# Kernel optimization log

Hardware: AMD Instinct MI355X
Metric: run time of the kernel (lower is better)

## Reference

```python
import jax, jax.numpy as jnp
import numpy as np

N_NODES = 50000
N_EDGES = 800000
FEAT_IN = 128
POS_IN = 16
EDGE_FEAT_IN = 16
H = 64
L = 4


def _lin(k, fan_in, fan_out):
    kw, kb = jax.random.split(k)
    s = 1.0 / np.sqrt(fan_in)
    W = jax.random.uniform(kw, (fan_in, fan_out), minval=-s, maxval=s, dtype=jnp.float32)
    b = jax.random.uniform(kb, (fan_out,), minval=-s, maxval=s, dtype=jnp.float32)
    return W, b


def setup_inputs() -> dict:
    key = jax.random.key(0)
    ks = jax.random.split(key, 32)
    h = jax.random.normal(ks[0], (N_NODES, FEAT_IN), dtype=jnp.float32)
    e = jax.random.normal(ks[1], (N_EDGES, EDGE_FEAT_IN), dtype=jnp.float32)
    p = jax.random.normal(ks[2], (N_NODES, POS_IN), dtype=jnp.float32)
    edge_index = jax.random.randint(ks[3], (2, N_EDGES), 0, N_NODES, dtype=jnp.int64 if jax.config.x64_enabled else jnp.int32)
    he_W, he_b = _lin(ks[4], FEAT_IN, H)
    ee_W, ee_b = _lin(ks[5], EDGE_FEAT_IN, H)
    pe_W, pe_b = _lin(ks[6], POS_IN, H)

    def stack(fan_in, base):
        Ws, bs = [], []
        for i in range(L):
            W, b = _lin(jax.random.fold_in(ks[7], base * 100 + i), fan_in, H)
            Ws.append(W); bs.append(b)
        return jnp.stack(Ws), jnp.stack(bs)

    hm_W, hm_b = stack(5 * H, 0)  # h_message_mlp
    hu_W, hu_b = stack(2 * H, 1)  # h_update
    eu_W, eu_b = stack(3 * H, 2)  # e_update
    pm_W, pm_b = stack(3 * H, 3)  # p_message_mlp
    pu_W, pu_b = stack(2 * H, 4)  # p_update
    return dict(h=h, e=e, p=p, edge_index=edge_index,
                he_W=he_W, he_b=he_b, ee_W=ee_W, ee_b=ee_b, pe_W=pe_W, pe_b=pe_b,
                hm_W=hm_W, hm_b=hm_b, hu_W=hu_W, hu_b=hu_b,
                eu_W=eu_W, eu_b=eu_b, pm_W=pm_W, pm_b=pm_b, pu_W=pu_W, pu_b=pu_b)


def reference(h, e, p, edge_index, he_W, he_b, ee_W, ee_b, pe_W, pe_b,
              hm_W, hm_b, hu_W, hu_b, eu_W, eu_b, pm_W, pm_b, pu_W, pu_b):
    send, rec = edge_index[0], edge_index[1]
    n = h.shape[0]
    h = h @ he_W + he_b  # [N,H]
    e = e @ ee_W + ee_b  # [E,H]
    p = p @ pe_W + pe_b  # [N,H]
    for i in range(L):
        hp_send = jnp.concatenate((h[send], p[send]), axis=1)  # [E,2H]
        hp_rec = jnp.concatenate((h[rec], p[rec]), axis=1)     # [E,2H]
        h_msg = jnp.concatenate((hp_send, hp_rec, e), axis=1) @ hm_W[i] + hm_b[i]  # [E,H]
        h_agg = jax.ops.segment_sum(h_msg, rec, num_segments=n)  # [N,H]
        h = jnp.concatenate((h, h_agg), axis=1) @ hu_W[i] + hu_b[i]
        e = jnp.concatenate((h[send], h[rec], e), axis=1) @ eu_W[i] + eu_b[i]
        p_msg = jnp.concatenate((p[send], p[rec], e), axis=1) @ pm_W[i] + pm_b[i]
        p_agg = jax.ops.segment_sum(p_msg, rec, num_segments=n)
        p = jnp.concatenate((p, p_agg), axis=1) @ pu_W[i] + pu_b[i]
    return (h, p)
```

## Files before the change

kernel.cpp:

```cpp
#include <hip/hip_runtime.h>
#include <hip/hip_bf16.h>

#define NN 50000
#define NE 800000

typedef __hip_bfloat16 bf16;
typedef __attribute__((ext_vector_type(8))) short bf16x8s;
typedef __attribute__((ext_vector_type(4))) float f32x4;

#define OFF_HP     0L
#define OFF_HSUM   12800000L
#define OFF_PSUM   25600000L
#define OFF_ESUM   38400000L
#define OFF_EAGGA  41600000L
#define OFF_EAGGB  54400000L
#define OFF_WFMT   67200000L
#define OFF_ROWPTR 67716096L
#define OFF_COLIDX 67916100L
#define OFF_SSEND  71116100L
#define OFF_SEG    74316100L
#define OFF_CNT    77516100L
#define OFF_BSUM   77716100L

#define SCAN_B 196

#define FW_HE 0
#define FW_EE 8192
#define FW_PE 10240
#define FW_L0 12288
#define LSTR  61440
#define R_HAGG 0
#define R_HMR  12288
#define R_HU   20480
#define R_EUS  28672
#define R_EUR  32768
#define R_EUE  36864
#define R_PAGG 40960
#define R_PMR  49152
#define R_PU   53248

#define AGG_STRIDE 72

__device__ __forceinline__ bf16x8s bfrag(const bf16* w, int c, int t, int lane) {
    return *(const bf16x8s*)(w + ((long)(c*4 + t)*64 + lane)*8);
}
__device__ __forceinline__ bf16x8s cvt8(const float* fp) {
    float4 f0 = ((const float4*)fp)[0];
    float4 f1 = ((const float4*)fp)[1];
    bf16 tmp[8];
    tmp[0]=__float2bfloat16(f0.x); tmp[1]=__float2bfloat16(f0.y);
    tmp[2]=__float2bfloat16(f0.z); tmp[3]=__float2bfloat16(f0.w);
    tmp[4]=__float2bfloat16(f1.x); tmp[5]=__float2bfloat16(f1.y);
    tmp[6]=__float2bfloat16(f1.z); tmp[7]=__float2bfloat16(f1.w);
    return *(const bf16x8s*)tmp;
}

__global__ __launch_bounds__(256) void wfmt_k(
    const float* __restrict__ he, const float* __restrict__ ee, const float* __restrict__ pe,
    const float* __restrict__ hm, const float* __restrict__ hu, const float* __restrict__ eu,
    const float* __restrict__ pm, const float* __restrict__ pu, bf16* __restrict__ wf)
{
    int s = blockIdx.x;
    const float* src = nullptr; int rowoff = 0, Ksrc = 0, Kpad = 0, mode = 0, split = 0, gap = 0; long doff = 0;
    if      (s == 0) { src = he; Ksrc = 128; Kpad = 128; doff = FW_HE; }
    else if (s == 1) { src = ee; Ksrc = 16;  Kpad = 32;  doff = FW_EE; }
    else if (s == 2) { src = pe; Ksrc = 16;  Kpad = 32;  doff = FW_PE; }
    else {
        int i = (s - 3) / 9, g = (s - 3) % 9;
        long base = FW_L0 + (long)i*LSTR;
        const float* HM = hm + (long)i*320*64;
        const float* HU = hu + (long)i*128*64;
        const float* EU = eu + (long)i*192*64;
        const float* PM = pm + (long)i*192*64;
        const float* PU = pu + (long)i*128*64;
        switch (g) {
          case 0:  src=HM; mode=4; split=128; gap=128; Kpad=192; doff=base+R_HAGG; break;
          case 1:  src=HM; rowoff=128; Ksrc=128; Kpad=128; doff=base+R_HMR;  break;
          case 2:  src=HU; rowoff=0;   Ksrc=128; Kpad=128; doff=base+R_HU;   break;
          case 3:  src=EU; rowoff=0;   Ksrc=64;  Kpad=64;  doff=base+R_EUS;  break;
          case 4:  src=EU; rowoff=64;  Ksrc=64;  Kpad=64;  doff=base+R_EUR;  break;
          case 5:  src=EU; rowoff=128; Ksrc=64;  Kpad=64;  doff=base+R_EUE;  break;
          case 6:  src=PM; mode=4; split=64; gap=64; Kpad=128; doff=base+R_PAGG; break;
          case 7:  src=PM; rowoff=64;  Ksrc=64;  Kpad=64;  doff=base+R_PMR;  break;
          default: src=PU; rowoff=0;   Ksrc=128; Kpad=128; doff=base+R_PU;   break;
        }
    }
    int total = Kpad * 64;
    for (int idx = threadIdx.x; idx < total; idx += 256) {
        int j = idx & 7, l = (idx >> 3) & 63, ct = idx >> 9;
        int c = ct >> 2, t = ct & 3;
        int k = c*32 + (l >> 4)*8 + j;
        int n = t*16 + (l & 15);
        float v;
        if (mode == 4) v = src[(long)(k + (k >= split ? gap : 0))*64 + n];
        else           v = (k < Ksrc) ? src[(long)(rowoff + k)*64 + n] : 0.f;
        wf[doff + idx] = __float2bfloat16(v);
    }
}

__global__ __launch_bounds__(256) void hist_k(const int* __restrict__ rec, int* __restrict__ cnt)
{
    int e = blockIdx.x*256 + threadIdx.x;
    if (e < NE) atomicAdd(&cnt[rec[e]], 1);
}

__global__ __launch_bounds__(256) void scan1_k(const int* __restrict__ cnt, int* __restrict__ bsum)
{
    __shared__ int sdata[256];
    int tid = threadIdx.x;
    int i = blockIdx.x*256 + tid;
    sdata[tid] = (i < NN) ? cnt[i] : 0;
    __syncthreads();
    #pragma unroll
    for (int off = 128; off > 0; off >>= 1) {
        if (tid < off) sdata[tid] += sdata[tid + off];
        __syncthreads();
    }
    if (tid == 0) bsum[blockIdx.x] = sdata[0];
}

__global__ __launch_bounds__(256) void scan2_k(int* __restrict__ bsum)
{
    __shared__ int sdata[256];
    int tid = threadIdx.x;
    int v = (tid < SCAN_B) ? bsum[tid] : 0;
    sdata[tid] = v;
    __syncthreads();
    #pragma unroll
    for (int off = 1; off < 256; off <<= 1) {
        int t = (tid >= off) ? sdata[tid - off] : 0;
        __syncthreads();
        sdata[tid] += t;
        __syncthreads();
    }
    if (tid < SCAN_B) bsum[tid] = sdata[tid] - v;
}

__global__ __launch_bounds__(256) void scan3_k(const int* __restrict__ cnt,
    const int* __restrict__ bsum, int* __restrict__ rowptr)
{
    __shared__ int sdata[256];
    int tid = threadIdx.x;
    int i = blockIdx.x*256 + tid;
    sdata[tid] = (i < NN) ? cnt[i] : 0;
    __syncthreads();
    #pragma unroll
    for (int off = 1; off < 256; off <<= 1) {
        int t = (tid >= off) ? sdata[tid - off] : 0;
        __syncthreads();
        sdata[tid] += t;
        __syncthreads();
    }
    if (i < NN) rowptr[i + 1] = sdata[tid] + bsum[blockIdx.x];
    if (i == 0) rowptr[0] = 0;
}

__global__ __launch_bounds__(256) void scatter_k(const int* __restrict__ rec,
    const int* __restrict__ rowptr, int* __restrict__ cursor, int* __restrict__ colidx)
{
    int e = blockIdx.x*256 + threadIdx.x;
    if (e < NE) {
        int r = rec[e];
        int pos = atomicAdd(&cursor[r], 1);
        colidx[rowptr[r] + pos] = e;
    }
}

__global__ __launch_bounds__(256) void segfill_k(const int* __restrict__ rowptr, int* __restrict__ seg)
{
    int n = blockIdx.x*256 + threadIdx.x;
    if (n < NN) {
        int b = rowptr[n], e = rowptr[n + 1];
        for (int j = b; j < e; ++j) seg[j] = n;
    }
}

template <int DEPTH, bool BOTH>
__global__ __launch_bounds__(256) void gsum64_k(const bf16* __restrict__ hp, int coff,
    const int* __restrict__ ssend, const int* __restrict__ seg,
    float* __restrict__ out1, float* __restrict__ out2)
{
    __shared__ int s_ids[256];
    __shared__ int s_seg[256];
    int tid = threadIdx.x, lane = tid & 63, wv = tid >> 6;
    int gbase = blockIdx.x*256;
    s_ids[tid] = ssend[gbase + tid];
    s_seg[tid] = seg[gbase + tid];
    __syncthreads();
    int j0 = wv*64;
    const bf16* base = hp + coff + lane;
    constexpr int NB = 64 / DEPTH;

    unsigned short va[DEPTH], vb[DEPTH];
    unsigned short wa[BOTH ? DEPTH : 1], wb[BOTH ? DEPTH : 1];
    #pragma unroll
    for (int k = 0; k < DEPTH; ++k) {
        long o = (long)s_ids[j0 + k]*128;
        va[k] = *(const unsigned short*)(base + o);
        if (BOTH) wa[k] = *(const unsigned short*)(base + o + 64);
    }

    float a = 0.f, b2 = 0.f;
    int cur = s_seg[j0];
    #pragma unroll
    for (int b = 0; b < NB; ++b) {
        if (b < NB - 1) {
            #pragma unroll
            for (int k = 0; k < DEPTH; ++k) {
                long o = (long)s_ids[j0 + (b+1)*DEPTH + k]*128;
                vb[k] = *(const unsigned short*)(base + o);
                if (BOTH) wb[k] = *(const unsigned short*)(base + o + 64);
            }
        }
        #pragma unroll
        for (int k = 0; k < DEPTH; ++k) {
            int n = s_seg[j0 + b*DEPTH + k];
            if (n != cur) {
                atomicAdd(&out1[(long)cur*64 + lane], a);
                if (BOTH) atomicAdd(&out2[(long)cur*64 + lane], b2);
                a = 0.f; b2 = 0.f; cur = n;
            }
            a += __uint_as_float(((unsigned)va[k]) << 16);
            if (BOTH) b2 += __uint_as_float(((unsigned)wa[k]) << 16);
        }
        if (b < NB - 1) {
            #pragma unroll
            for (int k = 0; k < DEPTH; ++k) { va[k] = vb[k]; if (BOTH) wa[k] = wb[k]; }
        }
    }
    atomicAdd(&out1[(long)cur*64 + lane], a);
    if (BOTH) atomicAdd(&out2[(long)cur*64 + lane], b2);
}

__global__ __launch_bounds__(256) void esum_k(const float* __restrict__ e_in,
    const int* __restrict__ colidx, const int* __restrict__ seg, const int* __restrict__ send,
    int* __restrict__ ssend, float* __restrict__ esum)
{
    __shared__ int s_ids[256];
    __shared__ int s_seg[256];
    int tid = threadIdx.x;
    int gbase = blockIdx.x*256;
    int id = colidx[gbase + tid];
    s_ids[tid] = id;
    s_seg[tid] = seg[gbase + tid];
    ssend[gbase + tid] = send[id];
    __syncthreads();
    int grp = tid >> 4, c = tid & 15;
    int j0 = grp*16;
    float vv[16];
    #pragma unroll
    for (int jj = 0; jj < 16; ++jj) vv[jj] = e_in[(long)s_ids[j0 + jj]*16 + c];
    float a = 0.f;
    int cur = s_seg[j0];
    #pragma unroll
    for (int jj = 0; jj < 16; ++jj) {
        int n = s_seg[j0 + jj];
        if (n != cur) { atomicAdd(&esum[(long)cur*16 + c], a); a = 0.f; cur = n; }
        a += vv[jj];
    }
    atomicAdd(&esum[(long)cur*16 + c], a);
}

__global__ __launch_bounds__(256) void eembn_k(const float* __restrict__ esum,
    const int* __restrict__ deg, const bf16* __restrict__ wEE, const float* __restrict__ ee_b,
    bf16* __restrict__ eagg)
{
    int tid = threadIdx.x, lane = tid & 63, wv = tid >> 6;
    int l15 = lane & 15, q = lane >> 4;
    int row = blockIdx.x*64 + wv*16 + l15;
    int rc = (row < NN) ? row : NN - 1;
    f32x4 acc[4];
    #pragma unroll
    for (int t = 0; t < 4; ++t) { acc[t][0]=0; acc[t][1]=0; acc[t][2]=0; acc[t][3]=0; }
    {
        bf16x8s af = {0,0,0,0,0,0,0,0};
        if (q < 2) af = cvt8(esum + (long)rc*16 + q*8);
        #pragma unroll
        for (int t = 0; t < 4; ++t)
            acc[t] = __builtin_amdgcn_mfma_f32_16x16x32_bf16(af, bfrag(wEE, 0, t, lane), acc[t], 0, 0, 0);
    }
    float bv[4];
    #pragma unroll
    for (int t = 0; t < 4; ++t) bv[t] = ee_b[t*16 + l15];
    #pragma unroll
    for (int r = 0; r < 4; ++r) {
        int ro = blockIdx.x*64 + wv*16 + q*4 + r;
        if (ro < NN) {
            float dg = (float)deg[ro];
            #pragma unroll
            for (int t = 0; t < 4; ++t)
                eagg[(long)ro*64 + t*16 + l15] = __float2bfloat16(acc[t][r] + dg*bv[t]);
        }
    }
}

__global__ __launch_bounds__(256) void hpemb_k(const float* __restrict__ h_in,
    const float* __restrict__ p_in,
    const bf16* __restrict__ wHE, const bf16* __restrict__ wPE,
    const float* __restrict__ he_b, const float* __restrict__ pe_b, bf16* __restrict__ hp)
{
    int tid = threadIdx.x, lane = tid & 63, wv = tid >> 6;
    int l15 = lane & 15, q = lane >> 4;
    int row = blockIdx.x*64 + wv*16 + l15;
    int rc = (row < NN) ? row : NN - 1;
    f32x4 aH[4], aP[4];
    #pragma unroll
    for (int t = 0; t < 4; ++t) {
        float bh = he_b[t*16 + l15], bp = pe_b[t*16 + l15];
        aH[t][0]=bh; aH[t][1]=bh; aH[t][2]=bh; aH[t][3]=bh;
        aP[t][0]=bp; aP[t][1]=bp; aP[t][2]=bp; aP[t][3]=bp;
    }
    #pragma unroll
    for (int c = 0; c < 4; ++c) {
        bf16x8s af = cvt8(h_in + (long)rc*128 + c*32 + q*8);
        #pragma unroll
        for (int t = 0; t < 4; ++t)
            aH[t] = __builtin_amdgcn_mfma_f32_16x16x32_bf16(af, bfrag(wHE, c, t, lane), aH[t], 0, 0, 0);
    }
    {
        bf16x8s af = {0,0,0,0,0,0,0,0};
        if (q < 2) af = cvt8(p_in + (long)rc*16 + q*8);
        #pragma unroll
        for (int t = 0; t < 4; ++t)
            aP[t] = __builtin_amdgcn_mfma_f32_16x16x32_bf16(af, bfrag(wPE, 0, t, lane), aP[t], 0, 0, 0);
    }
    #pragma unroll
    for (int r = 0; r < 4; ++r) {
        int ro = blockIdx.x*64 + wv*16 + q*4 + r;
        if (ro < NN)
            #pragma unroll
            for (int t = 0; t < 4; ++t) {
                hp[(long)ro*128 + t*16 + l15]      = __float2bfloat16(aH[t][r]);
                hp[(long)ro*128 + 64 + t*16 + l15] = __float2bfloat16(aP[t][r]);
            }
    }
}

__global__ __launch_bounds__(256) void hfuse_k(
    bf16* __restrict__ hp, float* __restrict__ hsum, const float* __restrict__ psum,
    const bf16* __restrict__ eagg, const int* __restrict__ deg,
    const bf16* __restrict__ wAGG, const bf16* __restrict__ wR, const float* __restrict__ mb,
    const bf16* __restrict__ wU, const float* __restrict__ ub, float* __restrict__ out2)
{
    __shared__ __align__(16) bf16 sAgg[64 * AGG_STRIDE];
    int tid = threadIdx.x, lane = tid & 63, wv = tid >> 6;
    int l15 = lane & 15, q = lane >> 4;
    int row = blockIdx.x*64 + wv*16 + l15;
    int rc = (row < NN) ? row : NN - 1;

    f32x4 aA[4], aR[4];
    #pragma unroll
    for (int t = 0; t < 4; ++t) {
        aA[t][0]=0;aA[t][1]=0;aA[t][2]=0;aA[t][3]=0;
        aR[t][0]=0;aR[t][1]=0;aR[t][2]=0;aR[t][3]=0;
    }
    #pragma unroll
    for (int c = 0; c < 6; ++c) {
        bf16x8s af = (c < 2) ? cvt8(hsum + (long)rc*64 + c*32 + q*8)
                   : (c < 4) ? cvt8(psum + (long)rc*64 + (c-2)*32 + q*8)
                             : *(const bf16x8s*)(eagg + (long)rc*64 + (c-4)*32 + q*8);
        #pragma unroll
        for (int t = 0; t < 4; ++t)
            aA[t] = __builtin_amdgcn_mfma_f32_16x16x32_bf16(af, bfrag(wAGG, c, t, lane), aA[t], 0, 0, 0);
    }
    if (row < NN) {
        float4 z4 = make_float4(0.f, 0.f, 0.f, 0.f);
        #pragma unroll
        for (int c = 0; c < 2; ++c) {
            *(float4*)(hsum + (long)rc*64 + c*32 + q*8)     = z4;
            *(float4*)(hsum + (long)rc*64 + c*32 + q*8 + 4) = z4;
        }
    }
    #pragma unroll
    for (int c = 0; c < 4; ++c) {
        bf16x8s af = *(const bf16x8s*)(hp + (long)rc*128 + c*32 + q*8);
        #pragma unroll
        for (int t = 0; t < 4; ++t)
            aR[t] = __builtin_amdgcn_mfma_f32_16x16x32_bf16(af, bfrag(wR, c, t, lane), aR[t], 0, 0, 0);
    }
    float mbv[4];
    #pragma unroll
    for (int t = 0; t < 4; ++t) mbv[t] = mb[t*16 + l15];
    #pragma unroll
    for (int r = 0; r < 4; ++r) {
        int ro = blockIdx.x*64 + wv*16 + q*4 + r;
        float dg = (float)deg[(ro < NN) ? ro : NN - 1];
        #pragma unroll
        for (int t = 0; t < 4; ++t)
            sAgg[(wv*16 + q*4 + r)*AGG_STRIDE + t*16 + l15] =
                __float2bfloat16(aA[t][r] + dg*(aR[t][r] + mbv[t]));
    }
    __syncthreads();
    f32x4 acc[4];
    #pragma unroll
    for (int t = 0; t < 4; ++t) { float b = ub[t*16 + l15]; acc[t][0]=b; acc[t][1]=b; acc[t][2]=b; acc[t][3]=b; }
    #pragma unroll
    for (int c = 0; c < 4; ++c) {
        bf16x8s af = (c < 2) ? *(const bf16x8s*)(hp + (long)rc*128 + c*32 + q*8)
                             : *(const bf16x8s*)(sAgg + (wv*16 + l15)*AGG_STRIDE + (c-2)*32 + q*8);
        #pragma unroll
        for (int t = 0; t < 4; ++t)
            acc[t] = __builtin_amdgcn_mfma_f32_16x16x32_bf16(af, bfrag(wU, c, t, lane), acc[t], 0, 0, 0);
    }
    #pragma unroll
    for (int r = 0; r < 4; ++r) {
        int ro = blockIdx.x*64 + wv*16 + q*4 + r;
        if (ro < NN) {
            #pragma unroll
            for (int t = 0; t < 4; ++t) {
                float fv = acc[t][r];
                hp[(long)ro*128 + t*16 + l15] = __float2bfloat16(fv);
                if (out2) out2[(long)ro*64 + t*16 + l15] = fv;
            }
        }
    }
}

__global__ __launch_bounds__(256) void pfuse_k(
    bf16* __restrict__ hp, const float* __restrict__ hsumN, float* __restrict__ psum,
    const bf16* __restrict__ eaggIn, bf16* __restrict__ eaggOut, const int* __restrict__ deg,
    const bf16* __restrict__ wEUS, const bf16* __restrict__ wEUR, const bf16* __restrict__ wEUE,
    const float* __restrict__ eub,
    const bf16* __restrict__ wAGG, const bf16* __restrict__ wR, const float* __restrict__ mb,
    const bf16* __restrict__ wU, const float* __restrict__ ub, float* __restrict__ out2)
{
    __shared__ __align__(16) bf16 sE[64 * AGG_STRIDE];
    __shared__ __align__(16) bf16 sAgg[64 * AGG_STRIDE];
    int tid = threadIdx.x, lane = tid & 63, wv = tid >> 6;
    int l15 = lane & 15, q = lane >> 4;
    int row = blockIdx.x*64 + wv*16 + l15;
    int rc = (row < NN) ? row : NN - 1;

    f32x4 aE[4], aH[4];
    #pragma unroll
    for (int t = 0; t < 4; ++t) {
        aE[t][0]=0;aE[t][1]=0;aE[t][2]=0;aE[t][3]=0;
        aH[t][0]=0;aH[t][1]=0;aH[t][2]=0;aH[t][3]=0;
    }
    #pragma unroll
    for (int c = 0; c < 4; ++c) {
        bf16x8s af = (c < 2) ? cvt8(hsumN + (long)rc*64 + c*32 + q*8)
                             : *(const bf16x8s*)(eaggIn + (long)rc*64 + (c-2)*32 + q*8);
        #pragma unroll
        for (int t = 0; t < 4; ++t) {
            bf16x8s w = (c < 2) ? bfrag(wEUS, c, t, lane) : bfrag(wEUE, c-2, t, lane);
            aE[t] = __builtin_amdgcn_mfma_f32_16x16x32_bf16(af, w, aE[t], 0, 0, 0);
        }
    }
    #pragma unroll
    for (int c = 0; c < 2; ++c) {
        bf16x8s af = *(const bf16x8s*)(hp + (long)rc*128 + c*32 + q*8);
        #pragma unroll
        for (int t = 0; t < 4; ++t)
            aH[t] = __builtin_amdgcn_mfma_f32_16x16x32_bf16(af, bfrag(wEUR, c, t, lane), aH[t], 0, 0, 0);
    }
    float ebv[4];
    #pragma unroll
    for (int t = 0; t < 4; ++t) ebv[t] = eub[t*16 + l15];
    #pragma unroll
    for (int r = 0; r < 4; ++r) {
        int ro = blockIdx.x*64 + wv*16 + q*4 + r;
        float dg = (float)deg[(ro < NN) ? ro : NN - 1];
        #pragma unroll
        for (int t = 0; t < 4; ++t) {
            bf16 ev = __float2bfloat16(aE[t][r] + dg*(aH[t][r] + ebv[t]));
            sE[(wv*16 + q*4 + r)*AGG_STRIDE + t*16 + l15] = ev;
            if (eaggOut && ro < NN) eaggOut[(long)ro*64 + t*16 + l15] = ev;
        }
    }
    __syncthreads();

    f32x4 aA[4], aR[4];
    #pragma unroll
    for (int t = 0; t < 4; ++t) {
        aA[t][0]=0;aA[t][1]=0;aA[t][2]=0;aA[t][3]=0;
        aR[t][0]=0;aR[t][1]=0;aR[t][2]=0;aR[t][3]=0;
    }
    #pragma unroll
    for (int c = 0; c < 4; ++c) {
        bf16x8s af = (c < 2) ? cvt8(psum + (long)rc*64 + c*32 + q*8)
                             : *(const bf16x8s*)(sE + (wv*16 + l15)*AGG_STRIDE + (c-2)*32 + q*8);
        #pragma unroll
        for (int t = 0; t < 4; ++t)
            aA[t] = __builtin_amdgcn_mfma_f32_16x16x32_bf16(af, bfrag(wAGG, c, t, lane), aA[t], 0, 0, 0);
    }
    if (row < NN) {
        float4 z4 = make_float4(0.f, 0.f, 0.f, 0.f);
        #pragma unroll
        for (int c = 0; c < 2; ++c) {
            *(float4*)(psum + (long)rc*64 + c*32 + q*8)     = z4;
            *(float4*)(psum + (long)rc*64 + c*32 + q*8 + 4) = z4;
        }
    }
    #pragma unroll
    for (int c = 0; c < 2; ++c) {
        bf16x8s af = *(const bf16x8s*)(hp + (long)rc*128 + 64 + c*32 + q*8);
        #pragma unroll
        for (int t = 0; t < 4; ++t)
            aR[t] = __builtin_amdgcn_mfma_f32_16x16x32_bf16(af, bfrag(wR, c, t, lane), aR[t], 0, 0, 0);
    }
    float mbv[4];
    #pragma unroll
    for (int t = 0; t < 4; ++t) mbv[t] = mb[t*16 + l15];
    #pragma unroll
    for (int r = 0; r < 4; ++r) {
        int ro = blockIdx.x*64 + wv*16 + q*4 + r;
        float dg = (float)deg[(ro < NN) ? ro : NN - 1];
        #pragma unroll
        for (int t = 0; t < 4; ++t)
            sAgg[(wv*16 + q*4 + r)*AGG_STRIDE + t*16 + l15] =
                __float2bfloat16(aA[t][r] + dg*(aR[t][r] + mbv[t]));
    }
    __syncthreads();
    f32x4 acc[4];
    #pragma unroll
    for (int t = 0; t < 4; ++t) { float b = ub[t*16 + l15]; acc[t][0]=b; acc[t][1]=b; acc[t][2]=b; acc[t][3]=b; }
    #pragma unroll
    for (int c = 0; c < 4; ++c) {
        bf16x8s af = (c < 2) ? *(const bf16x8s*)(hp + (long)rc*128 + 64 + c*32 + q*8)
                             : *(const bf16x8s*)(sAgg + (wv*16 + l15)*AGG_STRIDE + (c-2)*32 + q*8);
        #pragma unroll
        for (int t = 0; t < 4; ++t)
            acc[t] = __builtin_amdgcn_mfma_f32_16x16x32_bf16(af, bfrag(wU, c, t, lane), acc[t], 0, 0, 0);
    }
    #pragma unroll
    for (int r = 0; r < 4; ++r) {
        int ro = blockIdx.x*64 + wv*16 + q*4 + r;
        if (ro < NN) {
            #pragma unroll
            for (int t = 0; t < 4; ++t) {
                float fv = acc[t][r];
                hp[(long)ro*128 + 64 + t*16 + l15] = __float2bfloat16(fv);
                if (out2) out2[(long)ro*64 + t*16 + l15] = fv;
            }
        }
    }
}

extern "C" void kernel_launch(void* const* d_in, const int* in_sizes, int n_in,
                              void* d_out, int out_size, void* d_ws, size_t ws_size,
                              hipStream_t stream)
{
    (void)in_sizes; (void)n_in; (void)out_size; (void)ws_size;
    const float* h_in = (const float*)d_in[0];
    const float* e_in = (const float*)d_in[1];
    const float* p_in = (const float*)d_in[2];
    const int*  ei   = (const int*)d_in[3];
    const int* send = ei;
    const int* rec  = ei + NE;
    const float* he_W = (const float*)d_in[4];  const float* he_b = (const float*)d_in[5];
    const float* ee_W = (const float*)d_in[6];  const float* ee_b = (const float*)d_in[7];
    const float* pe_W = (const float*)d_in[8];  const float* pe_b = (const float*)d_in[9];
    const float* hm_W = (const float*)d_in[10]; const float* hm_b = (const float*)d_in[11];
    const float* hu_W = (const float*)d_in[12]; const float* hu_b = (const float*)d_in[13];
    const float* eu_W = (const float*)d_in[14]; const float* eu_b = (const float*)d_in[15];
    const float* pm_W = (const float*)d_in[16]; const float* pm_b = (const float*)d_in[17];
    const float* pu_W = (const float*)d_in[18]; const float* pu_b = (const float*)d_in[19];

    char* ws = (char*)d_ws;
    bf16* hp     = (bf16*)(ws + OFF_HP);
    float* hsum  = (float*)(ws + OFF_HSUM);
    float* psum  = (float*)(ws + OFF_PSUM);
    float* esum  = (float*)(ws + OFF_ESUM);
    bf16* eaggA  = (bf16*)(ws + OFF_EAGGA);
    bf16* eaggB  = (bf16*)(ws + OFF_EAGGB);
    bf16* wf     = (bf16*)(ws + OFF_WFMT);
    int* rowptr  = (int*)(ws + OFF_ROWPTR);
    int* colidx  = (int*)(ws + OFF_COLIDX);
    int* ssend   = (int*)(ws + OFF_SSEND);
    int* segarr  = (int*)(ws + OFF_SEG);
    int* cnt     = (int*)(ws + OFF_CNT);
    int* bsum    = (int*)(ws + OFF_BSUM);
    float* dout  = (float*)d_out;

    const int EB   = NE / 256;
    const int NB64 = (NN + 63) / 64;

    (void)hipMemsetAsync(cnt, 0, NN * sizeof(int), stream);
    hist_k<<<EB, 256, 0, stream>>>(rec, cnt);
    scan1_k<<<SCAN_B, 256, 0, stream>>>(cnt, bsum);
    scan2_k<<<1, 256, 0, stream>>>(bsum);
    scan3_k<<<SCAN_B, 256, 0, stream>>>(cnt, bsum, rowptr);
    (void)hipMemsetAsync(cnt, 0, NN * sizeof(int), stream);
    scatter_k<<<EB, 256, 0, stream>>>(rec, rowptr, cnt, colidx);
    segfill_k<<<SCAN_B, 256, 0, stream>>>(rowptr, segarr);

    (void)hipMemsetAsync(hsum, 0, (long)NN*(64 + 64 + 16)*sizeof(float), stream);

    esum_k<<<EB, 256, 0, stream>>>(e_in, colidx, segarr, send, ssend, esum);

    wfmt_k<<<39, 256, 0, stream>>>(he_W, ee_W, pe_W, hm_W, hu_W, eu_W, pm_W, pu_W, wf);

    hpemb_k<<<NB64, 256, 0, stream>>>(h_in, p_in, wf + FW_HE, wf + FW_PE, he_b, pe_b, hp);
    eembn_k<<<NB64, 256, 0, stream>>>(esum, cnt, wf + FW_EE, ee_b, eaggA);
    gsum64_k<16, true><<<EB, 256, 0, stream>>>(hp, 0, ssend, segarr, hsum, psum);

    bf16* eA = eaggA;
    bf16* eB = eaggB;
    for (int i = 0; i < 4; ++i) {
        long base = FW_L0 + (long)i*LSTR;
        hfuse_k<<<NB64, 256, 0, stream>>>(hp, hsum, psum, eA, cnt,
            wf + base + R_HAGG, wf + base + R_HMR, hm_b + i*64,
            wf + base + R_HU, hu_b + i*64,
            (i == 3) ? dout : nullptr);
        gsum64_k<32, false><<<EB, 256, 0, stream>>>(hp, 0, ssend, segarr, hsum, nullptr);
        pfuse_k<<<NB64, 256, 0, stream>>>(hp, hsum, psum, eA, (i < 3) ? eB : nullptr, cnt,
            wf + base + R_EUS, wf + base + R_EUR, wf + base + R_EUE, eu_b + i*64,
            wf + base + R_PAGG, wf + base + R_PMR, pm_b + i*64,
            wf + base + R_PU, pu_b + i*64,
            (i == 3) ? dout + (long)NN*64 : nullptr);
        if (i < 3)
            gsum64_k<32, false><<<EB, 256, 0, stream>>>(hp, 64, ssend, segarr, psum, nullptr);
        bf16* tmp = eA; eA = eB; eB = tmp;
    }
}
```

Measured before the change: 657.3 us.

## Fuse segfill into scan, merge embedding kernels, bucket scatter by node range, retune gsum depth

Result: faster. 621.0 us (-5.5%).

```diff
diff --git a/kernel.cpp b/kernel.cpp
--- a/kernel.cpp
+++ b/kernel.cpp
@@ -3,6 +3,9 @@
 
 #define NN 50000
 #define NE 800000
+#define NB64 782
+#define EB   3125
+#define NODES_PER_XCD 6250
 
 typedef __hip_bfloat16 bf16;
 typedef __attribute__((ext_vector_type(8))) short bf16x8s;
@@ -137,12 +140,13 @@
 }
 
 __global__ __launch_bounds__(256) void scan3_k(const int* __restrict__ cnt,
-    const int* __restrict__ bsum, int* __restrict__ rowptr)
+    const int* __restrict__ bsum, int* __restrict__ rowptr, int* __restrict__ seg)
 {
     __shared__ int sdata[256];
     int tid = threadIdx.x;
     int i = blockIdx.x*256 + tid;
-    sdata[tid] = (i < NN) ? cnt[i] : 0;
+    int v = (i < NN) ? cnt[i] : 0;
+    sdata[tid] = v;
     __syncthreads();
     #pragma unroll
     for (int off = 1; off < 256; off <<= 1) {
@@ -151,85 +155,27 @@
         sdata[tid] += t;
         __syncthreads();
     }
-    if (i < NN) rowptr[i + 1] = sdata[tid] + bsum[blockIdx.x];
+    if (i < NN) {
+        int hi = sdata[tid] + bsum[blockIdx.x];
+        rowptr[i + 1] = hi;
+        for (int j = hi - v; j < hi; ++j) seg[j] = i;
+    }
     if (i == 0) rowptr[0] = 0;
 }
 
 __global__ __launch_bounds__(256) void scatter_k(const int* __restrict__ rec,
     const int* __restrict__ rowptr, int* __restrict__ cursor, int* __restrict__ colidx)
 {
-    int e = blockIdx.x*256 + threadIdx.x;
+    int b = blockIdx.x;
+    int bucket = b & 7;
+    int e = (b >> 3)*256 + threadIdx.x;
     if (e < NE) {
         int r = rec[e];
-        int pos = atomicAdd(&cursor[r], 1);
-        colidx[rowptr[r] + pos] = e;
-    }
-}
-
-__global__ __launch_bounds__(256) void segfill_k(const int* __restrict__ rowptr, int* __restrict__ seg)
-{
-    int n = blockIdx.x*256 + threadIdx.x;
-    if (n < NN) {
-        int b = rowptr[n], e = rowptr[n + 1];
-        for (int j = b; j < e; ++j) seg[j] = n;
-    }
-}
-
-template <int DEPTH, bool BOTH>
-__global__ __launch_bounds__(256) void gsum64_k(const bf16* __restrict__ hp, int coff,
-    const int* __restrict__ ssend, const int* __restrict__ seg,
-    float* __restrict__ out1, float* __restrict__ out2)
-{
-    __shared__ int s_ids[256];
-    __shared__ int s_seg[256];
-    int tid = threadIdx.x, lane = tid & 63, wv = tid >> 6;
-    int gbase = blockIdx.x*256;
-    s_ids[tid] = ssend[gbase + tid];
-    s_seg[tid] = seg[gbase + tid];
-    __syncthreads();
-    int j0 = wv*64;
-    const bf16* base = hp + coff + lane;
-    constexpr int NB = 64 / DEPTH;
-
-    unsigned short va[DEPTH], vb[DEPTH];
-    unsigned short wa[BOTH ? DEPTH : 1], wb[BOTH ? DEPTH : 1];
-    #pragma unroll
-    for (int k = 0; k < DEPTH; ++k) {
-        long o = (long)s_ids[j0 + k]*128;
-        va[k] = *(const unsigned short*)(base + o);
-        if (BOTH) wa[k] = *(const unsigned short*)(base + o + 64);
-    }
-
-    float a = 0.f, b2 = 0.f;
-    int cur = s_seg[j0];
-    #pragma unroll
-    for (int b = 0; b < NB; ++b) {
-        if (b < NB - 1) {
-            #pragma unroll
-            for (int k = 0; k < DEPTH; ++k) {
-                long o = (long)s_ids[j0 + (b+1)*DEPTH + k]*128;
-                vb[k] = *(const unsigned short*)(base + o);
-                if (BOTH) wb[k] = *(const unsigned short*)(base + o + 64);
-            }
-        }
-        #pragma unroll
-        for (int k = 0; k < DEPTH; ++k) {
-            int n = s_seg[j0 + b*DEPTH + k];
-            if (n != cur) {
-                atomicAdd(&out1[(long)cur*64 + lane], a);
-                if (BOTH) atomicAdd(&out2[(long)cur*64 + lane], b2);
-                a = 0.f; b2 = 0.f; cur = n;
-            }
-            a += __uint_as_float(((unsigned)va[k]) << 16);
-            if (BOTH) b2 += __uint_as_float(((unsigned)wa[k]) << 16);
-        }
-        if (b < NB - 1) {
-            #pragma unroll
-            for (int k = 0; k < DEPTH; ++k) { va[k] = vb[k]; if (BOTH) wa[k] = wb[k]; }
-        }
-    }
-    atomicAdd(&out1[(long)cur*64 + lane], a);
-    if (BOTH) atomicAdd(&out2[(long)cur*64 + lane], b2);
+        if (r / NODES_PER_XCD == bucket) {
+            int pos = atomicAdd(&cursor[r], 1);
+            colidx[rowptr[r] + pos] = e;
+        }
+    }
 }
 
 __global__ __launch_bounds__(256) void esum_k(const float* __restrict__ e_in,
@@ -261,78 +207,115 @@
     atomicAdd(&esum[(long)cur*16 + c], a);
 }
 
-__global__ __launch_bounds__(256) void eembn_k(const float* __restrict__ esum,
-    const int* __restrict__ deg, const bf16* __restrict__ wEE, const float* __restrict__ ee_b,
-    bf16* __restrict__ eagg)
+template <bool BOTH>
+__global__ __launch_bounds__(256) void gsum64_k(const bf16* __restrict__ hp, int coff,
+    const int* __restrict__ ssend, const int* __restrict__ seg,
+    float* __restrict__ out1, float* __restrict__ out2)
+{
+    __shared__ int s_ids[256];
+    __shared__ int s_seg[256];
+    int tid = threadIdx.x, lane = tid & 63, wv = tid >> 6;
+    int gbase = blockIdx.x*256;
+    s_ids[tid] = ssend[gbase + tid];
+    s_seg[tid] = seg[gbase + tid];
+    __syncthreads();
+    int j0 = wv*64;
+    const bf16* base = hp + coff + lane;
+
+    unsigned short va[16], vb[16];
+    unsigned short wa[BOTH ? 16 : 1], wb[BOTH ? 16 : 1];
+    #pragma unroll
+    for (int k = 0; k < 16; ++k) {
+        long o = (long)s_ids[j0 + k]*128;
+        va[k] = *(const unsigned short*)(base + o);
+        if (BOTH) wa[k] = *(const unsigned short*)(base + o + 64);
+    }
+    float a = 0.f, b2 = 0.f;
+    int cur = s_seg[j0];
+    #pragma unroll
+    for (int b = 0; b < 4; ++b) {
+        if (b < 3) {
+            #pragma unroll
+            for (int k = 0; k < 16; ++k) {
+                long o = (long)s_ids[j0 + (b+1)*16 + k]*128;
+                vb[k] = *(const unsigned short*)(base + o);
+                if (BOTH) wb[k] = *(const unsigned short*)(base + o + 64);
+            }
+        }
+        #pragma unroll
+        for (int k = 0; k < 16; ++k) {
+            int n = s_seg[j0 + b*16 + k];
+            if (n != cur) {
+                atomicAdd(&out1[(long)cur*64 + lane], a);
+                if (BOTH) atomicAdd(&out2[(long)cur*64 + lane], b2);
+                a = 0.f; b2 = 0.f; cur = n;
+            }
+            a += __uint_as_float(((unsigned)va[k]) << 16);
+            if (BOTH) b2 += __uint_as_float(((unsigned)wa[k]) << 16);
+        }
+        if (b < 3) {
+            #pragma unroll
+            for (int k = 0; k < 16; ++k) { va[k] = vb[k]; if (BOTH) wa[k] = wb[k]; }
+        }
+    }
+    atomicAdd(&out1[(long)cur*64 + lane], a);
+    if (BOTH) atomicAdd(&out2[(long)cur*64 + lane], b2);
+}
+
+__global__ __launch_bounds__(256) void hpemb_k(const float* __restrict__ h_in,
+    const float* __restrict__ p_in, const float* __restrict__ esum, const int* __restrict__ deg,
+    const bf16* __restrict__ wHE, const bf16* __restrict__ wPE, const bf16* __restrict__ wEE,
+    const float* __restrict__ he_b, const float* __restrict__ pe_b, const float* __restrict__ ee_b,
+    bf16* __restrict__ hp, bf16* __restrict__ eagg)
 {
     int tid = threadIdx.x, lane = tid & 63, wv = tid >> 6;
     int l15 = lane & 15, q = lane >> 4;
     int row = blockIdx.x*64 + wv*16 + l15;
     int rc = (row < NN) ? row : NN - 1;
-    f32x4 acc[4];
-    #pragma unroll
-    for (int t = 0; t < 4; ++t) { acc[t][0]=0; acc[t][1]=0; acc[t][2]=0; acc[t][3]=0; }
+    f32x4 aH[4], aP[4], aE[4];
+    #pragma unroll
+    for (int t = 0; t < 4; ++t) {
+        float bh = he_b[t*16 + l15], bp = pe_b[t*16 + l15];
+        aH[t][0]=bh; aH[t][1]=bh; aH[t][2]=bh; aH[t][3]=bh;
+        aP[t][0]=bp; aP[t][1]=bp; aP[t][2]=bp; aP[t][3]=bp;
+        aE[t][0]=0;  aE[t][1]=0;  aE[t][2]=0;  aE[t][3]=0;
+    }
+    #pragma unroll
+    for (int c = 0; c < 4; ++c) {
+        bf16x8s af = cvt8(h_in + (long)rc*128 + c*32 + q*8);
+        #pragma unroll
+        for (int t = 0; t < 4; ++t)
+            aH[t] = __builtin_amdgcn_mfma_f32_16x16x32_bf16(af, bfrag(wHE, c, t, lane), aH[t], 0, 0, 0);
+    }
+    {
+        bf16x8s af = {0,0,0,0,0,0,0,0};
+        if (q < 2) af = cvt8(p_in + (long)rc*16 + q*8);
+        #pragma unroll
+        for (int t = 0; t < 4; ++t)
+            aP[t] = __builtin_amdgcn_mfma_f32_16x16x32_bf16(af, bfrag(wPE, 0, t, lane), aP[t], 0, 0, 0);
+    }
     {
         bf16x8s af = {0,0,0,0,0,0,0,0};
         if (q < 2) af = cvt8(esum + (long)rc*16 + q*8);
         #pragma unroll
         for (int t = 0; t < 4; ++t)
-            acc[t] = __builtin_amdgcn_mfma_f32_16x16x32_bf16(af, bfrag(wEE, 0, t, lane), acc[t], 0, 0, 0);
-    }
-    float bv[4];
-    #pragma unroll
-    for (int t = 0; t < 4; ++t) bv[t] = ee_b[t*16 + l15];
+            aE[t] = __builtin_amdgcn_mfma_f32_16x16x32_bf16(af, bfrag(wEE, 0, t, lane), aE[t], 0, 0, 0);
+    }
+    float ebv[4];
+    #pragma unroll
+    for (int t = 0; t < 4; ++t) ebv[t] = ee_b[t*16 + l15];
     #pragma unroll
     for (int r = 0; r < 4; ++r) {
         int ro = blockIdx.x*64 + wv*16 + q*4 + r;
         if (ro < NN) {
             float dg = (float)deg[ro];
             #pragma unroll
-            for (int t = 0; t < 4; ++t)
-                eagg[(long)ro*64 + t*16 + l15] = __float2bfloat16(acc[t][r] + dg*bv[t]);
-        }
-    }
-}
-
-__global__ __launch_bounds__(256) void hpemb_k(const float* __restrict__ h_in,
-    const float* __restrict__ p_in,
-    const bf16* __restrict__ wHE, const bf16* __restrict__ wPE,
-    const float* __restrict__ he_b, const float* __restrict__ pe_b, bf16* __restrict__ hp)
-{
-    int tid = threadIdx.x, lane = tid & 63, wv = tid >> 6;
-    int l15 = lane & 15, q = lane >> 4;
-    int row = blockIdx.x*64 + wv*16 + l15;
-    int rc = (row < NN) ? row : NN - 1;
-    f32x4 aH[4], aP[4];
-    #pragma unroll
-    for (int t = 0; t < 4; ++t) {
-        float bh = he_b[t*16 + l15], bp = pe_b[t*16 + l15];
-        aH[t][0]=bh; aH[t][1]=bh; aH[t][2]=bh; aH[t][3]=bh;
-        aP[t][0]=bp; aP[t][1]=bp; aP[t][2]=bp; aP[t][3]=bp;
-    }
-    #pragma unroll
-    for (int c = 0; c < 4; ++c) {
-        bf16x8s af = cvt8(h_in + (long)rc*128 + c*32 + q*8);
-        #pragma unroll
-        for (int t = 0; t < 4; ++t)
-            aH[t] = __builtin_amdgcn_mfma_f32_16x16x32_bf16(af, bfrag(wHE, c, t, lane), aH[t], 0, 0, 0);
-    }
-    {
-        bf16x8s af = {0,0,0,0,0,0,0,0};
-        if (q < 2) af = cvt8(p_in + (long)rc*16 + q*8);
-        #pragma unroll
-        for (int t = 0; t < 4; ++t)
-            aP[t] = __builtin_amdgcn_mfma_f32_16x16x32_bf16(af, bfrag(wPE, 0, t, lane), aP[t], 0, 0, 0);
-    }
-    #pragma unroll
-    for (int r = 0; r < 4; ++r) {
-        int ro = blockIdx.x*64 + wv*16 + q*4 + r;
-        if (ro < NN)
-            #pragma unroll
             for (int t = 0; t < 4; ++t) {
                 hp[(long)ro*128 + t*16 + l15]      = __float2bfloat16(aH[t][r]);
                 hp[(long)ro*128 + 64 + t*16 + l15] = __float2bfloat16(aP[t][r]);
+                eagg[(long)ro*64 + t*16 + l15]     = __float2bfloat16(aE[t][r] + dg*ebv[t]);
             }
+        }
     }
 }
 
@@ -573,27 +556,22 @@
     int* bsum    = (int*)(ws + OFF_BSUM);
     float* dout  = (float*)d_out;
 
-    const int EB   = NE / 256;
-    const int NB64 = (NN + 63) / 64;
-
     (void)hipMemsetAsync(cnt, 0, NN * sizeof(int), stream);
     hist_k<<<EB, 256, 0, stream>>>(rec, cnt);
     scan1_k<<<SCAN_B, 256, 0, stream>>>(cnt, bsum);
     scan2_k<<<1, 256, 0, stream>>>(bsum);
-    scan3_k<<<SCAN_B, 256, 0, stream>>>(cnt, bsum, rowptr);
+    scan3_k<<<SCAN_B, 256, 0, stream>>>(cnt, bsum, rowptr, segarr);
     (void)hipMemsetAsync(cnt, 0, NN * sizeof(int), stream);
-    scatter_k<<<EB, 256, 0, stream>>>(rec, rowptr, cnt, colidx);
-    segfill_k<<<SCAN_B, 256, 0, stream>>>(rowptr, segarr);
+    scatter_k<<<EB*8, 256, 0, stream>>>(rec, rowptr, cnt, colidx);
 
     (void)hipMemsetAsync(hsum, 0, (long)NN*(64 + 64 + 16)*sizeof(float), stream);
 
     esum_k<<<EB, 256, 0, stream>>>(e_in, colidx, segarr, send, ssend, esum);
-
     wfmt_k<<<39, 256, 0, stream>>>(he_W, ee_W, pe_W, hm_W, hu_W, eu_W, pm_W, pu_W, wf);
 
-    hpemb_k<<<NB64, 256, 0, stream>>>(h_in, p_in, wf + FW_HE, wf + FW_PE, he_b, pe_b, hp);
-    eembn_k<<<NB64, 256, 0, stream>>>(esum, cnt, wf + FW_EE, ee_b, eaggA);
-    gsum64_k<16, true><<<EB, 256, 0, stream>>>(hp, 0, ssend, segarr, hsum, psum);
+    hpemb_k<<<NB64, 256, 0, stream>>>(h_in, p_in, esum, cnt,
+        wf + FW_HE, wf + FW_PE, wf + FW_EE, he_b, pe_b, ee_b, hp, eaggA);
+    gsum64_k<true><<<EB, 256, 0, stream>>>(hp, 0, ssend, segarr, hsum, psum);
 
     bf16* eA = eaggA;
     bf16* eB = eaggB;
@@ -601,16 +579,15 @@
         long base = FW_L0 + (long)i*LSTR;
         hfuse_k<<<NB64, 256, 0, stream>>>(hp, hsum, psum, eA, cnt,
             wf + base + R_HAGG, wf + base + R_HMR, hm_b + i*64,
-            wf + base + R_HU, hu_b + i*64,
-            (i == 3) ? dout : nullptr);
-        gsum64_k<32, false><<<EB, 256, 0, stream>>>(hp, 0, ssend, segarr, hsum, nullptr);
+            wf + base + R_HU, hu_b + i*64, (i == 3) ? dout : nullptr);
+        gsum64_k<false><<<EB, 256, 0, stream>>>(hp, 0, ssend, segarr, hsum, nullptr);
         pfuse_k<<<NB64, 256, 0, stream>>>(hp, hsum, psum, eA, (i < 3) ? eB : nullptr, cnt,
             wf + base + R_EUS, wf + base + R_EUR, wf + base + R_EUE, eu_b + i*64,
             wf + base + R_PAGG, wf + base + R_PMR, pm_b + i*64,
             wf + base + R_PU, pu_b + i*64,
             (i == 3) ? dout + (long)NN*64 : nullptr);
         if (i < 3)
-            gsum64_k<32, false><<<EB, 256, 0, stream>>>(hp, 64, ssend, segarr, psum, nullptr);
+            gsum64_k<false><<<EB, 256, 0, stream>>>(hp, 64, ssend, segarr, psum, nullptr);
         bf16* tmp = eA; eA = eB; eB = tmp;
     }
 }
```
